# Kernel optimization log

Hardware: AMD Instinct MI355X
Metric: run time of the kernel (lower is better)

Reference implementation:

```python
import jax, jax.numpy as jnp
import numpy as np

N_NODES = 50000
N_EDGES = 800000
NODE_IN = 128
NODE_OUT = 64
EDGE_IN = 64
EDGE_OUT = 64
NEG_SLOPE = 0.01  # torch F.leaky_relu default


def setup_inputs() -> dict:
    key = jax.random.key(0)
    k = jax.random.split(key, 6)
    h = jax.random.normal(k[0], (N_NODES, NODE_IN), dtype=jnp.float32)
    e = jax.random.normal(k[1], (N_EDGES, EDGE_IN), dtype=jnp.float32)
    # Linear weights (bias=False), scaled roughly like torch default init
    Wn = jax.random.normal(k[2], (NODE_OUT, NODE_IN), dtype=jnp.float32) * (1.0 / np.sqrt(NODE_IN))
    We = jax.random.normal(k[3], (EDGE_OUT, EDGE_IN), dtype=jnp.float32) * (1.0 / np.sqrt(EDGE_IN))
    Wa = jax.random.normal(k[4], (1, EDGE_OUT + NODE_OUT), dtype=jnp.float32) * (1.0 / np.sqrt(EDGE_OUT + NODE_OUT))
    src = jax.random.randint(k[5], (N_EDGES,), 0, N_NODES, dtype=jnp.int32)
    return {"h": h, "e": e, "Wn": Wn, "We": We, "Wa": Wa, "src": src}


def reference(h, e, Wn, We, Wa, src):
    n_nodes = h.shape[0]
    node_feat = h @ Wn.T                         # [N, node_out] = fc_n(h)
    e_w = e @ We.T                               # [E, edge_out] = fc_e(e)
    src_ft = node_feat[src]                      # gather src node features per edge
    z2 = jnp.concatenate([e_w, src_ft], axis=-1) # [E, edge_out+node_out] (edge first, as in module)
    a = z2 @ Wa.T                                # [E, 1] attention logit
    e_lr = jnp.where(a >= 0, a, NEG_SLOPE * a)   # leaky_relu
    # segment softmax over edges grouped by src node (group_apply_edges softmax dim=1)
    m = jax.ops.segment_max(e_lr, src, num_segments=n_nodes)     # [N, 1]
    ex = jnp.exp(e_lr - m[src])
    denom = jax.ops.segment_sum(ex, src, num_segments=n_nodes)   # [N, 1]
    gamma = ex / denom[src]                      # [E, 1]
    e_weighted = gamma * e_w                     # [E, edge_out]
    return node_feat, e_weighted
```

## Files before the change

### kernel.cpp

```cpp
#include <hip/hip_runtime.h>


constexpr int kNodes   = 50000;
constexpr int kEdges   = 800000;
constexpr int kNodeIn  = 128;
constexpr int kNodeOut = 64;
constexpr int kEdgeIn  = 64;
constexpr int kEdgeOut = 64;
constexpr int kNodesP  = 50016;
#define NEG_SLOPE 0.01f

typedef __attribute__((ext_vector_type(8))) short short8;
typedef __attribute__((ext_vector_type(4))) short short4v;
typedef __attribute__((ext_vector_type(4))) float f32x4;

constexpr int kOffV     = 0;
constexpr int kOffSn    = 64;
constexpr int kOffDenom = 50064;
constexpr int kOffRep   = 100064;
constexpr int kOffEx    = 500192;
constexpr int kOffWeB   = 1300192;
constexpr int kOffWnB   = 1302240;
constexpr int kOffEbf   = 1306368;
constexpr int kRepTotal = 8 * kNodesP;

__device__ inline short f2bf(float x) {
    union { float f; unsigned u; } v; v.f = x;
    unsigned r = v.u + 0x7FFFu + ((v.u >> 16) & 1u);
    return (short)(r >> 16);
}

__global__ void k0_prep(const float* __restrict__ We, const float* __restrict__ Wn,
                        const float* __restrict__ Wa,
                        float* __restrict__ v, short* __restrict__ Web,
                        short* __restrict__ Wnb) {
    int b = blockIdx.x, t = threadIdx.x;
    if (b == 0 && t < kEdgeIn) {
        float acc = 0.f;
        #pragma unroll
        for (int c = 0; c < kEdgeOut; ++c) acc = fmaf(Wa[c], We[c * kEdgeIn + t], acc);
        v[t] = acc;
    }
    if (b < 16) {
        int i = b * 256 + t;
        Web[i] = f2bf(We[i]);
    } else {
        int i = (b - 16) * 256 + t;
        Wnb[i] = f2bf(Wn[i]);
    }
}

__global__ __launch_bounds__(256) void k1_mfma(
    const float* __restrict__ h, const short* __restrict__ Wnb,
    const float* __restrict__ Wa, float* __restrict__ node_feat,
    float* __restrict__ s_n, float* __restrict__ rep) {
    const int lane = threadIdx.x & 63;
    const int l15  = lane & 15;
    const int lhi  = lane >> 4;
    const int n0   = blockIdx.x * 64 + (threadIdx.x >> 6) * 16;

    int gid = blockIdx.x * 256 + threadIdx.x;
    if (gid < kRepTotal) rep[gid] = 0.f;
    int g2 = gid + 200192;
    if (g2 < kRepTotal) rep[g2] = 0.f;

    short8 Af[4][4];
    #pragma unroll
    for (int kt = 0; kt < 4; ++kt)
        #pragma unroll
        for (int ct = 0; ct < 4; ++ct)
            Af[kt][ct] = *reinterpret_cast<const short8*>(
                Wnb + (ct * 16 + l15) * kNodeIn + kt * 32 + lhi * 8);

    const int  arow   = n0 + l15;
    const bool rv     = arow < kNodes;
    const float* hrow = h + (size_t)arow * kNodeIn;

    f32x4 acc[4];
    #pragma unroll
    for (int ct = 0; ct < 4; ++ct) acc[ct] = (f32x4)(0.f);

    #pragma unroll
    for (int kt = 0; kt < 4; ++kt) {
        short8 bf;
        if (rv) {
            f32x4 t0 = __builtin_nontemporal_load(
                reinterpret_cast<const f32x4*>(hrow + kt * 32 + lhi * 8));
            f32x4 t1 = __builtin_nontemporal_load(
                reinterpret_cast<const f32x4*>(hrow + kt * 32 + lhi * 8 + 4));
            bf[0] = f2bf(t0[0]); bf[1] = f2bf(t0[1]); bf[2] = f2bf(t0[2]); bf[3] = f2bf(t0[3]);
            bf[4] = f2bf(t1[0]); bf[5] = f2bf(t1[1]); bf[6] = f2bf(t1[2]); bf[7] = f2bf(t1[3]);
        } else {
            #pragma unroll
            for (int j = 0; j < 8; ++j) bf[j] = 0;
        }
        #pragma unroll
        for (int ct = 0; ct < 4; ++ct)
            acc[ct] = __builtin_amdgcn_mfma_f32_16x16x32_bf16(Af[kt][ct], bf, acc[ct], 0, 0, 0);
    }

    float part = 0.f;
    #pragma unroll
    for (int ct = 0; ct < 4; ++ct) {
        f32x4 wa4 = *reinterpret_cast<const f32x4*>(Wa + 64 + ct * 16 + lhi * 4);
        part = fmaf(wa4[0], acc[ct][0], part);
        part = fmaf(wa4[1], acc[ct][1], part);
        part = fmaf(wa4[2], acc[ct][2], part);
        part = fmaf(wa4[3], acc[ct][3], part);
        if (rv)
            __builtin_nontemporal_store(acc[ct],
                reinterpret_cast<f32x4*>(node_feat + (size_t)arow * kNodeOut + ct * 16 + lhi * 4));
    }
    part += __shfl_xor(part, 16, 64);
    part += __shfl_xor(part, 32, 64);
    if (rv && lhi == 0) s_n[arow] = part;
}

__global__ __launch_bounds__(256) void kconv(
    const float* __restrict__ e, const float* __restrict__ v,
    const int* __restrict__ src, const float* __restrict__ s_n,
    float* __restrict__ rep, float* __restrict__ ex,
    short* __restrict__ ebf) {
    const int t   = threadIdx.x;
    const int q   = t & 15;
    const int rlo = t >> 4;
    const long base = (long)blockIdx.x * 64;
    float* myrep = rep + (blockIdx.x & 7) * kNodesP;

    f32x4 vv = *(reinterpret_cast<const f32x4*>(v) + q);

    #pragma unroll
    for (int it = 0; it < 4; ++it) {
        long r = base + it * 16 + rlo;
        f32x4 d = __builtin_nontemporal_load(
            reinterpret_cast<const f32x4*>(e + r * kEdgeIn) + q);
        float part = d[0] * vv[0] + d[1] * vv[1] + d[2] * vv[2] + d[3] * vv[3];
        part += __shfl_xor(part, 1, 64);
        part += __shfl_xor(part, 2, 64);
        part += __shfl_xor(part, 4, 64);
        part += __shfl_xor(part, 8, 64);
        short4v o;
        o[0] = f2bf(d[0]); o[1] = f2bf(d[1]); o[2] = f2bf(d[2]); o[3] = f2bf(d[3]);
        *reinterpret_cast<short4v*>(ebf + r * kEdgeIn + q * 4) = o;
        if (q == 0) {
            int s = src[r];
            float a = part + s_n[s];
            float lr = (a >= 0.f) ? a : NEG_SLOPE * a;
            float xe = __expf(lr);
            ex[r] = xe;
            atomicAdd(myrep + s, xe);
        }
    }
}

__global__ __launch_bounds__(256) void kred(
    const float* __restrict__ rep, float* __restrict__ denom) {
    int i = blockIdx.x * 256 + threadIdx.x;
    if (i >= kNodes) return;
    float s = 0.f;
    #pragma unroll
    for (int x = 0; x < 8; ++x) s += rep[x * kNodesP + i];
    denom[i] = s;
}

__global__ __launch_bounds__(256) void k4_mfma(
    const short* __restrict__ ebf, const short* __restrict__ Web,
    const int* __restrict__ src, const float* __restrict__ denom,
    const float* __restrict__ ex, float* __restrict__ oute) {
    const int wave = threadIdx.x >> 6;
    const int lane = threadIdx.x & 63;
    const int l15  = lane & 15;
    const int lhi  = lane >> 4;
    const long base = (long)blockIdx.x * 256 + wave * 64;

    short8 Af[2][4];
    #pragma unroll
    for (int kt = 0; kt < 2; ++kt)
        #pragma unroll
        for (int ct = 0; ct < 4; ++ct)
            Af[kt][ct] = *reinterpret_cast<const short8*>(
                Web + (ct * 16 + l15) * kEdgeIn + kt * 32 + lhi * 8);

    f32x4 acc[4][4];
    #pragma unroll
    for (int m = 0; m < 4; ++m)
        #pragma unroll
        for (int n = 0; n < 4; ++n) acc[m][n] = (f32x4)(0.f);

    #pragma unroll
    for (int m = 0; m < 4; ++m) {
        const short* erow = ebf + (base + m * 16 + l15) * kEdgeIn;
        #pragma unroll
        for (int kt = 0; kt < 2; ++kt) {
            short8 bf = *reinterpret_cast<const short8*>(erow + kt * 32 + lhi * 8);
            #pragma unroll
            for (int ct = 0; ct < 4; ++ct)
                acc[m][ct] = __builtin_amdgcn_mfma_f32_16x16x32_bf16(
                    Af[kt][ct], bf, acc[m][ct], 0, 0, 0);
        }
    }

    #pragma unroll
    for (int m = 0; m < 4; ++m) {
        const long edge = base + m * 16 + l15;
        int s = src[edge];
        float g = ex[edge] * __builtin_amdgcn_rcpf(denom[s]);
        #pragma unroll
        for (int ct = 0; ct < 4; ++ct) {
            f32x4 o = acc[m][ct] * g;
            __builtin_nontemporal_store(o,
                reinterpret_cast<f32x4*>(oute + edge * kEdgeOut + ct * 16 + lhi * 4));
        }
    }
}

extern "C" void kernel_launch(void* const* d_in, const int* in_sizes, int n_in,
                              void* d_out, int out_size, void* d_ws, size_t ws_size,
                              hipStream_t stream) {
    const float* h   = (const float*)d_in[0];
    const float* e   = (const float*)d_in[1];
    const float* Wn  = (const float*)d_in[2];
    const float* We  = (const float*)d_in[3];
    const float* Wa  = (const float*)d_in[4];
    const int*   src = (const int*)d_in[5];

    float* node_feat = (float*)d_out;
    float* oute      = (float*)d_out + (size_t)kNodes * kNodeOut;

    float* ws    = (float*)d_ws;
    float* v     = ws + kOffV;
    float* s_n   = ws + kOffSn;
    float* denom = ws + kOffDenom;
    float* rep   = ws + kOffRep;
    float* ex    = ws + kOffEx;
    short* Web   = (short*)(ws + kOffWeB);
    short* Wnb   = (short*)(ws + kOffWnB);
    short* ebf   = (short*)(ws + kOffEbf);

    k0_prep<<<48, 256, 0, stream>>>(We, Wn, Wa, v, Web, Wnb);
    k1_mfma<<<(kNodes + 63) / 64, 256, 0, stream>>>(h, Wnb, Wa, node_feat, s_n, rep);
    kconv<<<kEdges / 64, 256, 0, stream>>>(e, v, src, s_n, rep, ex, ebf);
    kred<<<(kNodes + 255) / 256, 256, 0, stream>>>(rep, denom);
    k4_mfma<<<kEdges / 256, 256, 0, stream>>>(ebf, Web, src, denom, ex, oute);
}
```

Measured before the change: 163.5 us.

## Fold weight prep into consumers and drop replicated atomic reduction buffers

Removes the weight-prep kernel: each consumer now converts Wn/We to bf16 on the fly and kconv recomputes the We·Wa projection per block with shuffles. The 8-way replicated denominator buffer and its reduction kernel are replaced by direct atomics into a single denom array zeroed in k1. Nontemporal load hints are also dropped. This cuts two launches and the rep zero/reduce traffic, at the cost of more atomic contention and redundant per-block weight work.

```diff
diff --git a/kernel.cpp b/kernel.cpp
--- a/kernel.cpp
+++ b/kernel.cpp
@@ -7,22 +7,16 @@
 constexpr int kNodeOut = 64;
 constexpr int kEdgeIn  = 64;
 constexpr int kEdgeOut = 64;
-constexpr int kNodesP  = 50016;
 #define NEG_SLOPE 0.01f
 
 typedef __attribute__((ext_vector_type(8))) short short8;
 typedef __attribute__((ext_vector_type(4))) short short4v;
 typedef __attribute__((ext_vector_type(4))) float f32x4;
 
-constexpr int kOffV     = 0;
-constexpr int kOffSn    = 64;
-constexpr int kOffDenom = 50064;
-constexpr int kOffRep   = 100064;
-constexpr int kOffEx    = 500192;
-constexpr int kOffWeB   = 1300192;
-constexpr int kOffWnB   = 1302240;
-constexpr int kOffEbf   = 1306368;
-constexpr int kRepTotal = 8 * kNodesP;
+constexpr int kOffSn    = 0;
+constexpr int kOffDenom = 50048;
+constexpr int kOffEx    = 100096;
+constexpr int kOffEbf   = 900096;
 
 __device__ inline short f2bf(float x) {
     union { float f; unsigned u; } v; v.f = x;
@@ -30,47 +24,31 @@
     return (short)(r >> 16);
 }
 
-__global__ void k0_prep(const float* __restrict__ We, const float* __restrict__ Wn,
-                        const float* __restrict__ Wa,
-                        float* __restrict__ v, short* __restrict__ Web,
-                        short* __restrict__ Wnb) {
-    int b = blockIdx.x, t = threadIdx.x;
-    if (b == 0 && t < kEdgeIn) {
-        float acc = 0.f;
-        #pragma unroll
-        for (int c = 0; c < kEdgeOut; ++c) acc = fmaf(Wa[c], We[c * kEdgeIn + t], acc);
-        v[t] = acc;
-    }
-    if (b < 16) {
-        int i = b * 256 + t;
-        Web[i] = f2bf(We[i]);
-    } else {
-        int i = (b - 16) * 256 + t;
-        Wnb[i] = f2bf(Wn[i]);
-    }
-}
-
 __global__ __launch_bounds__(256) void k1_mfma(
-    const float* __restrict__ h, const short* __restrict__ Wnb,
+    const float* __restrict__ h, const float* __restrict__ Wn,
     const float* __restrict__ Wa, float* __restrict__ node_feat,
-    float* __restrict__ s_n, float* __restrict__ rep) {
+    float* __restrict__ s_n, float* __restrict__ denom) {
     const int lane = threadIdx.x & 63;
     const int l15  = lane & 15;
     const int lhi  = lane >> 4;
     const int n0   = blockIdx.x * 64 + (threadIdx.x >> 6) * 16;
 
     int gid = blockIdx.x * 256 + threadIdx.x;
-    if (gid < kRepTotal) rep[gid] = 0.f;
-    int g2 = gid + 200192;
-    if (g2 < kRepTotal) rep[g2] = 0.f;
+    if (gid < kNodes) denom[gid] = 0.f;
 
     short8 Af[4][4];
     #pragma unroll
     for (int kt = 0; kt < 4; ++kt)
         #pragma unroll
-        for (int ct = 0; ct < 4; ++ct)
-            Af[kt][ct] = *reinterpret_cast<const short8*>(
-                Wnb + (ct * 16 + l15) * kNodeIn + kt * 32 + lhi * 8);
+        for (int ct = 0; ct < 4; ++ct) {
+            const float* wrow = Wn + (ct * 16 + l15) * kNodeIn + kt * 32 + lhi * 8;
+            f32x4 w0 = *reinterpret_cast<const f32x4*>(wrow);
+            f32x4 w1 = *reinterpret_cast<const f32x4*>(wrow + 4);
+            short8 af;
+            af[0] = f2bf(w0[0]); af[1] = f2bf(w0[1]); af[2] = f2bf(w0[2]); af[3] = f2bf(w0[3]);
+            af[4] = f2bf(w1[0]); af[5] = f2bf(w1[1]); af[6] = f2bf(w1[2]); af[7] = f2bf(w1[3]);
+            Af[kt][ct] = af;
+        }
 
     const int  arow   = n0 + l15;
     const bool rv     = arow < kNodes;
@@ -84,10 +62,8 @@
     for (int kt = 0; kt < 4; ++kt) {
         short8 bf;
         if (rv) {
-            f32x4 t0 = __builtin_nontemporal_load(
-                reinterpret_cast<const f32x4*>(hrow + kt * 32 + lhi * 8));
-            f32x4 t1 = __builtin_nontemporal_load(
-                reinterpret_cast<const f32x4*>(hrow + kt * 32 + lhi * 8 + 4));
+            f32x4 t0 = *reinterpret_cast<const f32x4*>(hrow + kt * 32 + lhi * 8);
+            f32x4 t1 = *reinterpret_cast<const f32x4*>(hrow + kt * 32 + lhi * 8 + 4);
             bf[0] = f2bf(t0[0]); bf[1] = f2bf(t0[1]); bf[2] = f2bf(t0[2]); bf[3] = f2bf(t0[3]);
             bf[4] = f2bf(t1[0]); bf[5] = f2bf(t1[1]); bf[6] = f2bf(t1[2]); bf[7] = f2bf(t1[3]);
         } else {
@@ -117,23 +93,37 @@
 }
 
 __global__ __launch_bounds__(256) void kconv(
-    const float* __restrict__ e, const float* __restrict__ v,
-    const int* __restrict__ src, const float* __restrict__ s_n,
-    float* __restrict__ rep, float* __restrict__ ex,
-    short* __restrict__ ebf) {
+    const float* __restrict__ e, const float* __restrict__ We,
+    const float* __restrict__ Wa, const int* __restrict__ src,
+    const float* __restrict__ s_n, float* __restrict__ denom,
+    float* __restrict__ ex, short* __restrict__ ebf) {
     const int t   = threadIdx.x;
     const int q   = t & 15;
     const int rlo = t >> 4;
+    const int hi  = (t >> 4) & 3;
     const long base = (long)blockIdx.x * 64;
-    float* myrep = rep + (blockIdx.x & 7) * kNodesP;
-
-    f32x4 vv = *(reinterpret_cast<const f32x4*>(v) + q);
+
+    f32x4 vv = (f32x4)(0.f);
+    #pragma unroll
+    for (int cc = 0; cc < 16; ++cc) {
+        int c = hi * 16 + cc;
+        float wac = Wa[c];
+        f32x4 w = *reinterpret_cast<const f32x4*>(We + c * kEdgeIn + q * 4);
+        vv[0] = fmaf(wac, w[0], vv[0]);
+        vv[1] = fmaf(wac, w[1], vv[1]);
+        vv[2] = fmaf(wac, w[2], vv[2]);
+        vv[3] = fmaf(wac, w[3], vv[3]);
+    }
+    #pragma unroll
+    for (int j = 0; j < 4; ++j) {
+        vv[j] += __shfl_xor(vv[j], 16, 64);
+        vv[j] += __shfl_xor(vv[j], 32, 64);
+    }
 
     #pragma unroll
     for (int it = 0; it < 4; ++it) {
         long r = base + it * 16 + rlo;
-        f32x4 d = __builtin_nontemporal_load(
-            reinterpret_cast<const f32x4*>(e + r * kEdgeIn) + q);
+        f32x4 d = *(reinterpret_cast<const f32x4*>(e + r * kEdgeIn) + q);
         float part = d[0] * vv[0] + d[1] * vv[1] + d[2] * vv[2] + d[3] * vv[3];
         part += __shfl_xor(part, 1, 64);
         part += __shfl_xor(part, 2, 64);
@@ -148,23 +138,13 @@
             float lr = (a >= 0.f) ? a : NEG_SLOPE * a;
             float xe = __expf(lr);
             ex[r] = xe;
-            atomicAdd(myrep + s, xe);
-        }
-    }
-}
-
-__global__ __launch_bounds__(256) void kred(
-    const float* __restrict__ rep, float* __restrict__ denom) {
-    int i = blockIdx.x * 256 + threadIdx.x;
-    if (i >= kNodes) return;
-    float s = 0.f;
-    #pragma unroll
-    for (int x = 0; x < 8; ++x) s += rep[x * kNodesP + i];
-    denom[i] = s;
+            atomicAdd(denom + s, xe);
+        }
+    }
 }
 
 __global__ __launch_bounds__(256) void k4_mfma(
-    const short* __restrict__ ebf, const short* __restrict__ Web,
+    const short* __restrict__ ebf, const float* __restrict__ We,
     const int* __restrict__ src, const float* __restrict__ denom,
     const float* __restrict__ ex, float* __restrict__ oute) {
     const int wave = threadIdx.x >> 6;
@@ -177,9 +157,15 @@
     #pragma unroll
     for (int kt = 0; kt < 2; ++kt)
         #pragma unroll
-        for (int ct = 0; ct < 4; ++ct)
-            Af[kt][ct] = *reinterpret_cast<const short8*>(
-                Web + (ct * 16 + l15) * kEdgeIn + kt * 32 + lhi * 8);
+        for (int ct = 0; ct < 4; ++ct) {
+            const float* wrow = We + (ct * 16 + l15) * kEdgeIn + kt * 32 + lhi * 8;
+            f32x4 w0 = *reinterpret_cast<const f32x4*>(wrow);
+            f32x4 w1 = *reinterpret_cast<const f32x4*>(wrow + 4);
+            short8 af;
+            af[0] = f2bf(w0[0]); af[1] = f2bf(w0[1]); af[2] = f2bf(w0[2]); af[3] = f2bf(w0[3]);
+            af[4] = f2bf(w1[0]); af[5] = f2bf(w1[1]); af[6] = f2bf(w1[2]); af[7] = f2bf(w1[3]);
+            Af[kt][ct] = af;
+        }
 
     f32x4 acc[4][4];
     #pragma unroll
@@ -228,18 +214,12 @@
     float* oute      = (float*)d_out + (size_t)kNodes * kNodeOut;
 
     float* ws    = (float*)d_ws;
-    float* v     = ws + kOffV;
     float* s_n   = ws + kOffSn;
     float* denom = ws + kOffDenom;
-    float* rep   = ws + kOffRep;
     float* ex    = ws + kOffEx;
-    short* Web   = (short*)(ws + kOffWeB);
-    short* Wnb   = (short*)(ws + kOffWnB);
     short* ebf   = (short*)(ws + kOffEbf);
 
-    k0_prep<<<48, 256, 0, stream>>>(We, Wn, Wa, v, Web, Wnb);
-    k1_mfma<<<(kNodes + 63) / 64, 256, 0, stream>>>(h, Wnb, Wa, node_feat, s_n, rep);
-    kconv<<<kEdges / 64, 256, 0, stream>>>(e, v, src, s_n, rep, ex, ebf);
-    kred<<<(kNodes + 255) / 256, 256, 0, stream>>>(rep, denom);
-    k4_mfma<<<kEdges / 256, 256, 0, stream>>>(ebf, Web, src, denom, ex, oute);
-}
+    k1_mfma<<<(kNodes + 63) / 64, 256, 0, stream>>>(h, Wn, Wa, node_feat, s_n, denom);
+    kconv<<<kEdges / 64, 256, 0, stream>>>(e, We, Wa, src, s_n, denom, ex, ebf);
+    k4_mfma<<<kEdges / 256, 256, 0, stream>>>(ebf, We, src, denom, ex, oute);
+}
```

Result: slower. 197.9 us (+21.1%).

## Atomically accumulate softmax denominators directly, dropping replicated buffers and reduction kernel

Applied to the files above, without the earlier changes.

Replaces the 8-way replicated denominator buffers and the separate reduction kernel with direct atomicAdd into a single denom array, which k1 now zeroes. This removes one kernel launch plus the zeroing and reading of a 400K-float replica buffer. The cost is more atomic contention on each node's single address. The nontemporal loads of h and e are also replaced with plain loads.

```diff
diff --git a/kernel.cpp b/kernel.cpp
--- a/kernel.cpp
+++ b/kernel.cpp
@@ -7,7 +7,6 @@
 constexpr int kNodeOut = 64;
 constexpr int kEdgeIn  = 64;
 constexpr int kEdgeOut = 64;
-constexpr int kNodesP  = 50016;
 #define NEG_SLOPE 0.01f
 
 typedef __attribute__((ext_vector_type(8))) short short8;
@@ -17,12 +16,10 @@
 constexpr int kOffV     = 0;
 constexpr int kOffSn    = 64;
 constexpr int kOffDenom = 50064;
-constexpr int kOffRep   = 100064;
-constexpr int kOffEx    = 500192;
-constexpr int kOffWeB   = 1300192;
-constexpr int kOffWnB   = 1302240;
-constexpr int kOffEbf   = 1306368;
-constexpr int kRepTotal = 8 * kNodesP;
+constexpr int kOffEx    = 100064;
+constexpr int kOffWeB   = 900064;
+constexpr int kOffWnB   = 902112;
+constexpr int kOffEbf   = 906240;
 
 __device__ inline short f2bf(float x) {
     union { float f; unsigned u; } v; v.f = x;
@@ -53,16 +50,14 @@
 __global__ __launch_bounds__(256) void k1_mfma(
     const float* __restrict__ h, const short* __restrict__ Wnb,
     const float* __restrict__ Wa, float* __restrict__ node_feat,
-    float* __restrict__ s_n, float* __restrict__ rep) {
+    float* __restrict__ s_n, float* __restrict__ denom) {
     const int lane = threadIdx.x & 63;
     const int l15  = lane & 15;
     const int lhi  = lane >> 4;
     const int n0   = blockIdx.x * 64 + (threadIdx.x >> 6) * 16;
 
     int gid = blockIdx.x * 256 + threadIdx.x;
-    if (gid < kRepTotal) rep[gid] = 0.f;
-    int g2 = gid + 200192;
-    if (g2 < kRepTotal) rep[g2] = 0.f;
+    if (gid < kNodes) denom[gid] = 0.f;
 
     short8 Af[4][4];
     #pragma unroll
@@ -84,10 +79,8 @@
     for (int kt = 0; kt < 4; ++kt) {
         short8 bf;
         if (rv) {
-            f32x4 t0 = __builtin_nontemporal_load(
-                reinterpret_cast<const f32x4*>(hrow + kt * 32 + lhi * 8));
-            f32x4 t1 = __builtin_nontemporal_load(
-                reinterpret_cast<const f32x4*>(hrow + kt * 32 + lhi * 8 + 4));
+            f32x4 t0 = *reinterpret_cast<const f32x4*>(hrow + kt * 32 + lhi * 8);
+            f32x4 t1 = *reinterpret_cast<const f32x4*>(hrow + kt * 32 + lhi * 8 + 4);
             bf[0] = f2bf(t0[0]); bf[1] = f2bf(t0[1]); bf[2] = f2bf(t0[2]); bf[3] = f2bf(t0[3]);
             bf[4] = f2bf(t1[0]); bf[5] = f2bf(t1[1]); bf[6] = f2bf(t1[2]); bf[7] = f2bf(t1[3]);
         } else {
@@ -119,21 +112,19 @@
 __global__ __launch_bounds__(256) void kconv(
     const float* __restrict__ e, const float* __restrict__ v,
     const int* __restrict__ src, const float* __restrict__ s_n,
-    float* __restrict__ rep, float* __restrict__ ex,
+    float* __restrict__ denom, float* __restrict__ ex,
     short* __restrict__ ebf) {
     const int t   = threadIdx.x;
     const int q   = t & 15;
     const int rlo = t >> 4;
     const long base = (long)blockIdx.x * 64;
-    float* myrep = rep + (blockIdx.x & 7) * kNodesP;
 
     f32x4 vv = *(reinterpret_cast<const f32x4*>(v) + q);
 
     #pragma unroll
     for (int it = 0; it < 4; ++it) {
         long r = base + it * 16 + rlo;
-        f32x4 d = __builtin_nontemporal_load(
-            reinterpret_cast<const f32x4*>(e + r * kEdgeIn) + q);
+        f32x4 d = *(reinterpret_cast<const f32x4*>(e + r * kEdgeIn) + q);
         float part = d[0] * vv[0] + d[1] * vv[1] + d[2] * vv[2] + d[3] * vv[3];
         part += __shfl_xor(part, 1, 64);
         part += __shfl_xor(part, 2, 64);
@@ -148,19 +139,9 @@
             float lr = (a >= 0.f) ? a : NEG_SLOPE * a;
             float xe = __expf(lr);
             ex[r] = xe;
-            atomicAdd(myrep + s, xe);
-        }
-    }
-}
-
-__global__ __launch_bounds__(256) void kred(
-    const float* __restrict__ rep, float* __restrict__ denom) {
-    int i = blockIdx.x * 256 + threadIdx.x;
-    if (i >= kNodes) return;
-    float s = 0.f;
-    #pragma unroll
-    for (int x = 0; x < 8; ++x) s += rep[x * kNodesP + i];
-    denom[i] = s;
+            atomicAdd(denom + s, xe);
+        }
+    }
 }
 
 __global__ __launch_bounds__(256) void k4_mfma(
@@ -231,15 +212,13 @@
     float* v     = ws + kOffV;
     float* s_n   = ws + kOffSn;
     float* denom = ws + kOffDenom;
-    float* rep   = ws + kOffRep;
     float* ex    = ws + kOffEx;
     short* Web   = (short*)(ws + kOffWeB);
     short* Wnb   = (short*)(ws + kOffWnB);
     short* ebf   = (short*)(ws + kOffEbf);
 
     k0_prep<<<48, 256, 0, stream>>>(We, Wn, Wa, v, Web, Wnb);
-    k1_mfma<<<(kNodes + 63) / 64, 256, 0, stream>>>(h, Wnb, Wa, node_feat, s_n, rep);
-    kconv<<<kEdges / 64, 256, 0, stream>>>(e, v, src, s_n, rep, ex, ebf);
-    kred<<<(kNodes + 255) / 256, 256, 0, stream>>>(rep, denom);
+    k1_mfma<<<(kNodes + 63) / 64, 256, 0, stream>>>(h, Wnb, Wa, node_feat, s_n, denom);
+    kconv<<<kEdges / 64, 256, 0, stream>>>(e, v, src, s_n, denom, ex, ebf);
     k4_mfma<<<kEdges / 256, 256, 0, stream>>>(ebf, Web, src, denom, ex, oute);
 }
```

Measured after the change: 159.7 us. -2.3%, faster.
